# Optimization experiments

Hardware: AMD Instinct MI355X
Metric: run time of the kernel (lower is better)

## Reference

```python
import jax, jax.numpy as jnp
import numpy as np

KH, KW = 3, 3
STRIDE = (1, 1)
PAD = ((1, 1), (1, 1))
WEIGHT_BIT = 8


def asym_quant_params(num_bits, smin, smax):
    # ZeroQ asymmetric_linear_quantization_params (signed, integral zero point)
    n = 2.0 ** num_bits - 1.0
    scale = n / jnp.maximum(smax - smin, 1e-8)
    zero_point = jnp.round(scale * smin) + 2.0 ** (num_bits - 1)
    return scale, zero_point


def setup_inputs() -> dict:
    key = jax.random.key(0)
    k1, k2, k3 = jax.random.split(key, 3)
    x = jax.random.normal(k1, (16, 128, 56, 56), dtype=jnp.float32)
    weight = jax.random.normal(k2, (128, 128, 3, 3), dtype=jnp.float32) * 0.05
    bias = jax.random.normal(k3, (128,), dtype=jnp.float32) * 0.1
    return {"x": x, "weight": weight, "bias": bias, "activation_bit": 8}


def reference(x, weight, bias, activation_bit):
    B, C, H, W = x.shape
    Cout = weight.shape[0]

    # nn.functional.unfold(x, 3, stride=1, padding=1).transpose(1, 2)
    # conv_general_dilated_patches emits feature dim ordered (c, kh, kw),
    # matching torch unfold's channel-major layout.
    patches = jax.lax.conv_general_dilated_patches(
        x, filter_shape=(KH, KW), window_strides=STRIDE, padding=PAD)
    _, F, OH, OW = patches.shape          # F = C*KH*KW
    L = OH * OW
    calc_x = patches.reshape(B, F, L).transpose(0, 2, 1)  # [B, L, F]

    # ----- weight quantization: per-output-channel asymmetric int8 -----
    w2 = weight.reshape(Cout, -1)                          # [Cout, F]
    w_min = w2.min(axis=1)
    w_max = w2.max(axis=1)
    scale_w, zp_w = asym_quant_params(WEIGHT_BIT, w_min, w_max)  # [Cout]
    nw = 2.0 ** (WEIGHT_BIT - 1)
    qw = jnp.clip(jnp.round(scale_w[:, None] * w2 - zp_w[:, None]), -nw, nw - 1)

    # ----- activation quantization: per-tensor asymmetric -----
    x_min = calc_x.min()
    x_max = calc_x.max()
    scale_x, zp_x = asym_quant_params(activation_bit, x_min, x_max)
    nx = 2.0 ** (activation_bit - 1)
    qx = jnp.clip(jnp.round(scale_x * calc_x - zp_x), -nx, nx - 1)  # [B, L, F]

    # bias: linear_quantize(bias, scale_w*scale_x, 0)
    qb = jnp.round(scale_w * scale_x * bias)                # [Cout]

    # integer matmul + asymmetric zero-point correction
    # real value r ~= (q + zp) / scale, so
    # x.w*sx*sw = qx.qw + zp_w*sum(qx) + zp_x*sum(qw) + K*zp_w*zp_x
    mult_res = jnp.einsum('blf,of->blo', qx, qw)            # [B, L, Cout]
    K = w2.shape[1]
    res = (mult_res
           + zp_w * qx.sum(-1, keepdims=True)               # [B, L, 1]*[Cout]
           + zp_x * qw.sum(axis=1)                          # [Cout]
           + K * zp_w * zp_x
           + qb)                                            # [B, L, Cout]

    # requantize accumulator to activation_bit bits, then dequantize
    r_min, r_max = res.min(), res.max()
    scale_r, zp_r = asym_quant_params(activation_bit, r_min, r_max)
    nr = 2.0 ** (activation_bit - 1)
    qr = jnp.clip(jnp.round(scale_r * res - zp_r), -nr, nr - 1)
    out = (qr + zp_r) / scale_r / (scale_w * scale_x)       # [B, L, Cout]

    return out.transpose(0, 2, 1)                           # [B, Cout, L]
```

## Files before the change

### kernel.cpp

```cpp
#include <hip/hip_runtime.h>
#include <stdint.h>

#pragma clang fp contract(off)

typedef __attribute__((ext_vector_type(4))) int i32x4;
typedef __attribute__((ext_vector_type(16))) int i32x16;

#define B_    16
#define C_    128
#define HW_   56
#define L_    3136
#define CO_   128
#define F_    1152
#define M_    50176
#define NT_   784

#define OFF_PBMIN 0
#define OFF_PBMAX 3136
#define OFF_PRMIN 6272
#define OFF_PRMAX 9408
#define OFF_SW    12544
#define OFF_ZPW   13056
#define OFF_SXZX  13568
#define OFF_CNT   14080
#define OFF_QS    15616
#define OFF_QW    16384
#define OFF_QX    163840
#define OFF_S     6586368
#define OFF_RES   6787072

__device__ __forceinline__ int read_abit(const int* p) {
    int i = *p;
    if (i > 0 && i < 32) return i;
    float f = __int_as_float(i);
    int fi = (int)f;
    return (fi > 0 && fi < 32) ? fi : 8;
}

__device__ __forceinline__ int swz_tile(int blk) {
    return (blk & 7) * 98 + (blk >> 3);
}

__device__ __forceinline__ void gsync(char* ws, int sp) {
    unsigned* base = (unsigned*)(ws + OFF_CNT) + sp * 128;
    __syncthreads();
    if (threadIdx.x == 0) {
        __threadfence();
        atomicAdd(&base[(blockIdx.x & 7) * 16], 1u);
    }
    if (threadIdx.x < 8) {
        while (__hip_atomic_load(&base[threadIdx.x * 16],
                                 __ATOMIC_RELAXED, __HIP_MEMORY_SCOPE_AGENT) < 98u)
            __builtin_amdgcn_s_sleep(2);
    }
    __threadfence();
    __syncthreads();
}

__device__ __forceinline__ void block_fminmax(float& mn, float& mx, float* sred) {
    for (int m = 32; m; m >>= 1) {
        mn = fminf(mn, __shfl_xor(mn, m));
        mx = fmaxf(mx, __shfl_xor(mx, m));
    }
    int w = threadIdx.x >> 6;
    if ((threadIdx.x & 63) == 0) { sred[w] = mn; sred[4 + w] = mx; }
    __syncthreads();
    mn = fminf(fminf(sred[0], sred[1]), fminf(sred[2], sred[3]));
    mx = fmaxf(fmaxf(sred[4], sred[5]), fmaxf(sred[6], sred[7]));
    __syncthreads();
}
__device__ __forceinline__ void block_iminmax(int& mn, int& mx, int* ired) {
    for (int m = 32; m; m >>= 1) {
        mn = min(mn, __shfl_xor(mn, m));
        mx = max(mx, __shfl_xor(mx, m));
    }
    int w = threadIdx.x >> 6;
    if ((threadIdx.x & 63) == 0) { ired[w] = mn; ired[4 + w] = mx; }
    __syncthreads();
    mn = min(min(ired[0], ired[1]), min(ired[2], ired[3]));
    mx = max(max(ired[4], ired[5]), max(ired[6], ired[7]));
    __syncthreads();
}
__device__ __forceinline__ int block_isum(int v, int* ired) {
    for (int m = 32; m; m >>= 1) v += __shfl_xor(v, m);
    int w = threadIdx.x >> 6;
    if ((threadIdx.x & 63) == 0) ired[w] = v;
    __syncthreads();
    v = ired[0] + ired[1] + ired[2] + ired[3];
    __syncthreads();
    return v;
}

__global__ __launch_bounds__(256) void kA1(const float4* __restrict__ x4,
                                           char* __restrict__ ws) {
    __shared__ float sred[8];
    float mn = 0.0f, mx = 0.0f;
    int base = blockIdx.x * blockDim.x + threadIdx.x;
    int stride = NT_ * 256;
    #pragma unroll
    for (int k = 0; k < 8; ++k) {
        float4 v = x4[base + k * stride];
        mn = fminf(mn, fminf(fminf(v.x, v.y), fminf(v.z, v.w)));
        mx = fmaxf(mx, fmaxf(fmaxf(v.x, v.y), fmaxf(v.z, v.w)));
    }
    block_fminmax(mn, mx, sred);
    if (threadIdx.x == 0) {
        ((float*)(ws + OFF_PBMIN))[blockIdx.x] = mn;
        ((float*)(ws + OFF_PBMAX))[blockIdx.x] = mx;
    }
}

__global__ __launch_bounds__(256) void kA2(const float* __restrict__ wgt,
                                           const int* __restrict__ abit_p,
                                           char* __restrict__ ws) {
    __shared__ float sred[8];
    __shared__ int ired[8];
    if (blockIdx.x == CO_) {
        const float* pbmin = (const float*)(ws + OFF_PBMIN);
        const float* pbmax = (const float*)(ws + OFF_PBMAX);
        float mn = 0.0f, mx = 0.0f;
        for (int i = threadIdx.x; i < NT_; i += 256) {
            mn = fminf(mn, pbmin[i]);
            mx = fmaxf(mx, pbmax[i]);
        }
        block_fminmax(mn, mx, sred);
        if (threadIdx.x == 0) {
            int abit = read_abit(abit_p);
            float nlv = (float)((1 << abit) - 1);
            float sx = nlv / fmaxf(mx - mn, 1e-8f);
            float zx = rintf(sx * mn) + (float)(1 << (abit - 1));
            ((float*)(ws + OFF_SXZX))[0] = sx;
            ((float*)(ws + OFF_SXZX))[1] = zx;
        }
        return;
    }
    int o = blockIdx.x;
    const float* wr = wgt + o * F_;
    float mn = 3.4e38f, mx = -3.4e38f;
    for (int f = threadIdx.x; f < F_; f += 256) {
        float v = wr[f];
        mn = fminf(mn, v); mx = fmaxf(mx, v);
    }
    block_fminmax(mn, mx, sred);
    float sw = 255.0f / fmaxf(mx - mn, 1e-8f);
    float zw = rintf(sw * mn) + 128.0f;
    signed char* qw = (signed char*)(ws + OFF_QW);
    int qsum = 0;
    for (int f = threadIdx.x; f < F_; f += 256) {
        float q = fminf(fmaxf(rintf(sw * wr[f] - zw), -128.0f), 127.0f);
        int qi = (int)q;
        qsum += qi;
        int c = f / 9, j = f - c * 9;
        qw[j * 16384 + (c >> 4) * 2048 + (o << 4) + (c & 15)] = (signed char)qi;
    }
    qsum = block_isum(qsum, ired);
    if (threadIdx.x == 0) {
        ((int*)(ws + OFF_QS))[o]  = qsum;
        ((int*)(ws + OFF_ZPW))[o] = (int)zw;
        ((float*)(ws + OFF_SW))[o] = sw;
    }
}

__device__ __forceinline__ void dev_p2x(const float* __restrict__ x, char* ws, char* pool,
                                        float sx, float zx, int nx) {
    int (*ssum)[64] = (int(*)[64])pool;
    float lo = -(float)nx, hif = (float)(nx - 1);
    signed char* qxt = (signed char*)(ws + OFF_QX);
    int gid = swz_tile(blockIdx.x);
    int b = gid / 49, lcq = gid - b * 49;
    int l0 = lcq * 64;
    int t = threadIdx.x, lane = t & 63, cgp = t >> 6;
    int l = l0 + lane;
    const float* xb = x + ((size_t)b * C_) * L_ + l;
    int4* dst = (int4*)(qxt + ((size_t)(b * L_ + l)) * 128);
    int psum = 0;
    #pragma unroll
    for (int ii = 0; ii < 2; ++ii) {
        int c16 = (cgp + 4 * ii) * 16;
        int wds[4];
        #pragma unroll
        for (int k = 0; k < 4; ++k) {
            int wv = 0;
            #pragma unroll
            for (int e = 0; e < 4; ++e) {
                int c = c16 + 4 * k + e;
                float v = xb[(size_t)c * L_];
                int qi = (int)fminf(fmaxf(rintf(sx * v - zx), lo), hif);
                psum += qi;
                wv |= (qi & 255) << (8 * e);
            }
            wds[k] = wv;
        }
        int4 vv; vv.x = wds[0]; vv.y = wds[1]; vv.z = wds[2]; vv.w = wds[3];
        dst[c16 >> 4] = vv;
    }
    ssum[cgp][lane] = psum;
    __syncthreads();
    if (cgp == 0) {
        int* S = (int*)(ws + OFF_S);
        S[b * L_ + l] = ssum[0][lane] + ssum[1][lane] + ssum[2][lane] + ssum[3][lane];
    }
    __syncthreads();
}

template <bool WRITE_RES>
__device__ __forceinline__ void dev_p3(char* __restrict__ ws, char* pool, int* ired,
                                       const float* __restrict__ bias,
                                       int abit, float sx, float zx,
                                       i32x16& acc0, i32x16& acc1) {
    signed char* As = (signed char*)pool;
    signed char* Bs = (signed char*)(pool + 8192);
    int* S_s = (int*)(pool + 24576);
    int* sq  = (int*)(pool + 25504);
    const signed char* qxt = (const signed char*)(ws + OFF_QX);
    const signed char* qw  = (const signed char*)(ws + OFF_QW);
    const int* Sg  = (const int*)(ws + OFF_S);
    const int* zpw = (const int*)(ws + OFF_ZPW);

    int t = threadIdx.x;
    int mg = swz_tile(blockIdx.x) * 64;
    int b = mg / L_, l0 = mg - b * L_;
    int prow0 = l0 / HW_;
    int nx = 1 << (abit - 1);
    int q0 = min(max(-(int)zx, -nx), nx - 1);
    int pw = (q0 & 255) * 0x01010101;
    int4 pad4; pad4.x = pw; pad4.y = pw; pad4.z = pw; pad4.w = pw;
    int padS = C_ * q0;
    const signed char* qxtb = qxt + (size_t)b * L_ * 128;
    const int* Sb = Sg + b * L_;

    int chA = t & 7, rowA0 = t >> 3, rowA1 = rowA0 + 32;
    int li0 = l0 + rowA0, li1 = l0 + rowA1;
    int oh0 = li0 / HW_, ow0 = li0 - oh0 * HW_;
    int oh1 = li1 / HW_, ow1 = li1 - oh1 * HW_;

    int4 a0, a1, br0, br1, br2, br3;
    #define P3_LOAD_A(J) do {                                                          \
        int kh = (J) / 3 - 1, kw = (J) % 3 - 1;                                        \
        int ih = oh0 + kh, iw = ow0 + kw;                                              \
        a0 = ((unsigned)ih < HW_ && (unsigned)iw < HW_)                                \
             ? *(const int4*)(qxtb + ((ih * HW_ + iw) << 7) + (chA << 4)) : pad4;      \
        ih = oh1 + kh; iw = ow1 + kw;                                                  \
        a1 = ((unsigned)ih < HW_ && (unsigned)iw < HW_)                                \
             ? *(const int4*)(qxtb + ((ih * HW_ + iw) << 7) + (chA << 4)) : pad4;      \
    } while (0)
    #define P3_LOAD_B(J) do {                                                          \
        const int4* src = (const int4*)(qw + (J) * 16384);                             \
        br0 = src[t]; br1 = src[256 + t]; br2 = src[512 + t]; br3 = src[768 + t];      \
    } while (0)

    P3_LOAD_A(0); P3_LOAD_B(0);
    if (t < 232) {
        int ri = t / 58, c1 = t - ri * 58;
        int ih = prow0 - 1 + ri, iw = c1 - 1;
        S_s[t] = ((unsigned)ih < HW_ && (unsigned)iw < HW_) ? Sb[ih * HW_ + iw] : padS;
    }
    __syncthreads();
    if (t < 64) {
        int l = l0 + t;
        int oh = l / HW_, ow = l - oh * HW_;
        int ri = oh - prow0 + 1, ci = ow + 1;
        int s = 0;
        #pragma unroll
        for (int dr = -1; dr <= 1; ++dr)
            #pragma unroll
            for (int dc = -1; dc <= 1; ++dc)
                s += S_s[(ri + dr) * 58 + ci + dc];
        sq[t] = s;
    }

    int lane = t & 63, w = t >> 6;
    int wm = (w >> 1) << 5, wn = (w & 1) << 6;
    int r = lane & 31, hi = lane >> 5;
    #pragma unroll
    for (int i = 0; i < 16; ++i) { acc0[i] = 0; acc1[i] = 0; }

    #pragma unroll
    for (int j = 0; j < 9; ++j) {
        if (j > 0) __syncthreads();
        *(int4*)&As[(rowA0 << 7) + ((chA ^ (rowA0 & 7)) << 4)] = a0;
        *(int4*)&As[(rowA1 << 7) + ((chA ^ (rowA1 & 7)) << 4)] = a1;
        {
            int4* d = (int4*)Bs;
            d[t] = br0; d[256 + t] = br1; d[512 + t] = br2; d[768 + t] = br3;
        }
        if (j < 8) { P3_LOAD_A(j + 1); P3_LOAD_B(j + 1); }
        __syncthreads();
        i32x4 af[4], bf0[4], bf1[4];
        #pragma unroll
        for (int kk = 0; kk < 4; ++kk) {
            int ch2 = kk * 2 + hi, row = wm + r;
            af[kk]  = *(const i32x4*)&As[(row << 7) + ((ch2 ^ (row & 7)) << 4)];
            bf0[kk] = *(const i32x4*)&Bs[ch2 * 2048 + ((wn + r) << 4)];
            bf1[kk] = *(const i32x4*)&Bs[ch2 * 2048 + ((wn + 32 + r) << 4)];
        }
        #pragma unroll
        for (int kk = 0; kk < 4; ++kk) {
            acc0 = __builtin_amdgcn_mfma_i32_32x32x32_i8(af[kk], bf0[kk], acc0, 0, 0, 0);
            acc1 = __builtin_amdgcn_mfma_i32_32x32x32_i8(af[kk], bf1[kk], acc1, 0, 0, 0);
        }
    }
    #undef P3_LOAD_A
    #undef P3_LOAD_B

    int o0 = wn + r, o1 = wn + 32 + r;
    const int* qs = (const int*)(ws + OFF_QS);
    const float* swp = (const float*)(ws + OFF_SW);
    int zxi = (int)zx;
    int zw0 = zpw[o0], zw1 = zpw[o1];
    int c0 = zxi * qs[o0] + F_ * zw0 * zxi + (int)rintf(swp[o0] * sx * bias[o0]);
    int c1 = zxi * qs[o1] + F_ * zw1 * zxi + (int)rintf(swp[o1] * sx * bias[o1]);
    int lmin = INT32_MAX, lmax = INT32_MIN;
    int* resp = (int*)(ws + OFF_RES);
    #pragma unroll
    for (int g = 0; g < 16; ++g) {
        int row = wm + (g & 3) + ((g >> 2) << 3) + (hi << 2);
        int s = sq[row];
        int v0 = acc0[g] + zw0 * s + c0;
        int v1 = acc1[g] + zw1 * s + c1;
        acc0[g] = v0; acc1[g] = v1;
        lmin = min(lmin, min(v0, v1));
        lmax = max(lmax, max(v0, v1));
        if (WRITE_RES) {
            int m = mg + row;
            resp[m * CO_ + o0] = v0;
            resp[m * CO_ + o1] = v1;
        }
    }
    block_iminmax(lmin, lmax, ired);
    if (t == 0) {
        ((int*)(ws + OFF_PRMIN))[blockIdx.x] = lmin;
        ((int*)(ws + OFF_PRMAX))[blockIdx.x] = lmax;
    }
    __syncthreads();
}

__device__ __forceinline__ void dev_reduce_pr(const char* ws, int* ired,
                                              int& rmin, int& rmax) {
    const int* prmin = (const int*)(ws + OFF_PRMIN);
    const int* prmax = (const int*)(ws + OFF_PRMAX);
    int mn = INT32_MAX, mx = INT32_MIN;
    for (int i = threadIdx.x; i < NT_; i += 256) {
        mn = min(mn, prmin[i]);
        mx = max(mx, prmax[i]);
    }
    block_iminmax(mn, mx, ired);
    rmin = mn; rmax = mx;
}

__device__ __forceinline__ void dev_p4(const char* ws, char* pool, float* __restrict__ out,
                                       int abit, float sx, int rmin, int rmax,
                                       const i32x16& acc0, const i32x16& acc1) {
    const float* scale_w = (const float*)(ws + OFF_SW);
    float* tile = (float*)pool;
    int t = threadIdx.x;
    int mg = swz_tile(blockIdx.x) * 64;
    int b = mg / L_, l0 = mg - b * L_;
    int lane = t & 63, w = t >> 6;
    int wm = (w >> 1) << 5, wn = (w & 1) << 6;
    int r = lane & 31, hi = lane >> 5;
    int o0 = wn + r, o1 = wn + 32 + r;
    int nx = 1 << (abit - 1);
    float nlev = (float)((1 << abit) - 1);
    float rminf = (float)rmin, rmaxf = (float)rmax;
    float sr = nlev / fmaxf(rmaxf - rminf, 1e-8f);
    float zr = rintf(sr * rminf) + (float)nx;
    float lo = -(float)nx, hiq = (float)(nx - 1);
    float swsx0 = scale_w[o0] * sx, swsx1 = scale_w[o1] * sx;
    #pragma unroll
    for (int g = 0; g < 16; ++g) {
        int row = wm + (g & 3) + ((g >> 2) << 3) + (hi << 2);
        float qa = fminf(fmaxf(rintf(sr * (float)acc0[g] - zr), lo), hiq);
        float qb = fminf(fmaxf(rintf(sr * (float)acc1[g] - zr), lo), hiq);
        tile[row * 129 + o0] = ((qa + zr) / sr) / swsx0;
        tile[row * 129 + o1] = ((qb + zr) / sr) / swsx1;
    }
    __syncthreads();
    #pragma unroll
    for (int i = 0; i < 8; ++i) {
        int o = (t >> 4) + i * 16;
        int l4 = (t & 15) * 4;
        float4 f;
        #pragma unroll
        for (int jj = 0; jj < 4; ++jj)
            ((float*)&f)[jj] = tile[(l4 + jj) * 129 + o];
        *(float4*)(out + ((size_t)(b * CO_ + o)) * L_ + l0 + l4) = f;
    }
}

__global__ __launch_bounds__(256, 4) void kB(const float* __restrict__ x,
                                             const float* __restrict__ bias,
                                             const int* __restrict__ abit_p,
                                             char* __restrict__ ws,
                                             float* __restrict__ out) {
    __shared__ __align__(16) char pool[33280];
    __shared__ int ired[8];

    float sx = ((const float*)(ws + OFF_SXZX))[0];
    float zx = ((const float*)(ws + OFF_SXZX))[1];
    int abit = read_abit(abit_p);
    int nx = 1 << (abit - 1);

    dev_p2x(x, ws, pool, sx, zx, nx);
    gsync(ws, 0);

    i32x16 acc0, acc1;
    dev_p3<false>(ws, pool, ired, bias, abit, sx, zx, acc0, acc1);
    gsync(ws, 1);

    int rmin, rmax;
    dev_reduce_pr(ws, ired, rmin, rmax);
    dev_p4(ws, pool, out, abit, sx, rmin, rmax, acc0, acc1);
}

__global__ __launch_bounds__(256) void fbB1(const float* __restrict__ x,
                                            const int* __restrict__ abit_p,
                                            char* __restrict__ ws) {
    __shared__ __align__(16) char pool[1024];
    float sx = ((const float*)(ws + OFF_SXZX))[0];
    float zx = ((const float*)(ws + OFF_SXZX))[1];
    int abit = read_abit(abit_p);
    int nx = 1 << (abit - 1);
    dev_p2x(x, ws, pool, sx, zx, nx);
}

__global__ __launch_bounds__(256, 4) void fbB2(const float* __restrict__ bias,
                                               const int* __restrict__ abit_p,
                                               char* __restrict__ ws) {
    __shared__ __align__(16) char pool[25760];
    __shared__ int ired[8];
    float sx = ((const float*)(ws + OFF_SXZX))[0];
    float zx = ((const float*)(ws + OFF_SXZX))[1];
    int abit = read_abit(abit_p);
    i32x16 acc0, acc1;
    dev_p3<true>(ws, pool, ired, bias, abit, sx, zx, acc0, acc1);
}

__global__ __launch_bounds__(256) void fbB3(const int* __restrict__ abit_p,
                                            char* __restrict__ ws,
                                            float* __restrict__ out) {
    __shared__ int tile[64 * 65];
    __shared__ int ired[8];
    float sxv = ((const float*)(ws + OFF_SXZX))[0];
    int abit = read_abit(abit_p);
    float nlv = (float)((1 << abit) - 1);
    int rmin, rmax;
    dev_reduce_pr(ws, ired, rmin, rmax);

    const int* res = (const int*)(ws + OFF_RES);
    const float* scale_w = (const float*)(ws + OFF_SW);
    int t = threadIdx.x;
    int bid = blockIdx.x;
    int lcq = bid % 49; int tmp2 = bid / 49; int ocq = tmp2 & 1; int b = tmp2 >> 1;
    int l0 = lcq * 64, o0 = ocq * 64;

    const int* resb = res + ((size_t)(b * L_ + l0)) * CO_ + o0;
    #pragma unroll
    for (int i = 0; i < 4; ++i) {
        int lr = (t >> 4) + i * 16;
        int oc4 = (t & 15) * 4;
        int4 v = *(const int4*)(resb + lr * CO_ + oc4);
        int* d = &tile[lr * 65 + oc4];
        d[0] = v.x; d[1] = v.y; d[2] = v.z; d[3] = v.w;
    }
    int nxq = 1 << (abit - 1);
    float rminf = (float)rmin, rmaxf = (float)rmax;
    float sr = nlv / fmaxf(rmaxf - rminf, 1e-8f);
    float zr = rintf(sr * rminf) + (float)nxq;
    float lo = -(float)nxq, hiq = (float)(nxq - 1);
    __syncthreads();
    #pragma unroll
    for (int i = 0; i < 4; ++i) {
        int o = (t >> 4) + i * 16;
        int l4 = (t & 15) * 4;
        float swsx = scale_w[o0 + o] * sxv;
        float4 f;
        #pragma unroll
        for (int jj = 0; jj < 4; ++jj) {
            int rv = tile[(l4 + jj) * 65 + o];
            float q = fminf(fmaxf(rintf(sr * (float)rv - zr), lo), hiq);
            ((float*)&f)[jj] = ((q + zr) / sr) / swsx;
        }
        *(float4*)(out + ((size_t)(b * CO_ + o0 + o)) * L_ + l0 + l4) = f;
    }
}


extern "C" void kernel_launch(void* const* d_in, const int* in_sizes, int n_in,
                              void* d_out, int out_size, void* d_ws, size_t ws_size,
                              hipStream_t stream) {
    const float* x      = (const float*)d_in[0];
    const float* weight = (const float*)d_in[1];
    const float* bias   = (const float*)d_in[2];
    const int*   abit   = (const int*)d_in[3];
    float* out = (float*)d_out;
    char* ws = (char*)d_ws;

    int dev = 0;
    hipGetDevice(&dev);
    int ncu = 0;
    hipDeviceGetAttribute(&ncu, hipDeviceAttributeMultiprocessorCount, dev);
    int nb = 0;
    hipOccupancyMaxActiveBlocksPerMultiprocessor(&nb, (const void*)kB, 256, 0);

    kA1<<<NT_, 256, 0, stream>>>((const float4*)x, ws);
    kA2<<<CO_ + 1, 256, 0, stream>>>(weight, abit, ws);

    if (nb > 0 && (long)nb * (long)ncu >= NT_) {
        hipMemsetAsync(ws + OFF_CNT, 0, 1024, stream);
        kB<<<NT_, 256, 0, stream>>>(x, bias, abit, ws, out);
    } else {
        fbB1<<<NT_, 256, 0, stream>>>(x, abit, ws);
        fbB2<<<NT_, 256, 0, stream>>>(bias, abit, ws);
        fbB3<<<1568, 256, 0, stream>>>(abit, ws, out);
    }
}
```

Measured before the change: 54.63 us.

## Merge stats kernels and move activation quantization out of cooperative kernel

Merges the activation min/max kernel and the weight quantization kernel into a single launch. The final activation reduction now runs redundantly in every block of a separate quantize-x kernel. That kernel-boundary split replaces the first software grid barrier inside the persistent kernel, so the cooperative kernel holds only the GEMM and the dequant phase with one barrier. The exchange is an extra kernel launch plus 784 redundant reductions over 784 partials, in return for one fewer spin barrier and one fewer launch.

```diff
diff --git a/kernel.cpp b/kernel.cpp
--- a/kernel.cpp
+++ b/kernel.cpp
@@ -16,18 +16,18 @@
 #define NT_   784
 
 #define OFF_PBMIN 0
-#define OFF_PBMAX 3136
-#define OFF_PRMIN 6272
-#define OFF_PRMAX 9408
-#define OFF_SW    12544
-#define OFF_ZPW   13056
-#define OFF_SXZX  13568
-#define OFF_CNT   14080
-#define OFF_QS    15616
-#define OFF_QW    16384
-#define OFF_QX    163840
-#define OFF_S     6586368
-#define OFF_RES   6787072
+#define OFF_PBMAX 4096
+#define OFF_PRMIN 8192
+#define OFF_PRMAX 12288
+#define OFF_SW    16384
+#define OFF_ZPW   16896
+#define OFF_SXZX  17408
+#define OFF_CNT   17536
+#define OFF_QS    18048
+#define OFF_QW    18560
+#define OFF_QX    166016
+#define OFF_S     6588544
+#define OFF_RES   6789248
 
 __device__ __forceinline__ int read_abit(const int* p) {
     int i = *p;
@@ -41,8 +41,8 @@
     return (blk & 7) * 98 + (blk >> 3);
 }
 
-__device__ __forceinline__ void gsync(char* ws, int sp) {
-    unsigned* base = (unsigned*)(ws + OFF_CNT) + sp * 128;
+__device__ __forceinline__ void gsync(char* ws) {
+    unsigned* base = (unsigned*)(ws + OFF_CNT);
     __syncthreads();
     if (threadIdx.x == 0) {
         __threadfence();
@@ -91,50 +91,30 @@
     return v;
 }
 
-__global__ __launch_bounds__(256) void kA1(const float4* __restrict__ x4,
-                                           char* __restrict__ ws) {
-    __shared__ float sred[8];
-    float mn = 0.0f, mx = 0.0f;
-    int base = blockIdx.x * blockDim.x + threadIdx.x;
-    int stride = NT_ * 256;
-    #pragma unroll
-    for (int k = 0; k < 8; ++k) {
-        float4 v = x4[base + k * stride];
-        mn = fminf(mn, fminf(fminf(v.x, v.y), fminf(v.z, v.w)));
-        mx = fmaxf(mx, fmaxf(fmaxf(v.x, v.y), fmaxf(v.z, v.w)));
-    }
-    block_fminmax(mn, mx, sred);
-    if (threadIdx.x == 0) {
-        ((float*)(ws + OFF_PBMIN))[blockIdx.x] = mn;
-        ((float*)(ws + OFF_PBMAX))[blockIdx.x] = mx;
-    }
-}
-
-__global__ __launch_bounds__(256) void kA2(const float* __restrict__ wgt,
-                                           const int* __restrict__ abit_p,
-                                           char* __restrict__ ws) {
+__global__ __launch_bounds__(256) void kA(const float4* __restrict__ x4,
+                                          const float* __restrict__ wgt,
+                                          char* __restrict__ ws) {
     __shared__ float sred[8];
     __shared__ int ired[8];
-    if (blockIdx.x == CO_) {
-        const float* pbmin = (const float*)(ws + OFF_PBMIN);
-        const float* pbmax = (const float*)(ws + OFF_PBMAX);
+    int blk = blockIdx.x;
+    if (blk < NT_) {
         float mn = 0.0f, mx = 0.0f;
-        for (int i = threadIdx.x; i < NT_; i += 256) {
-            mn = fminf(mn, pbmin[i]);
-            mx = fmaxf(mx, pbmax[i]);
+        int base = blk * blockDim.x + threadIdx.x;
+        int stride = NT_ * 256;
+        #pragma unroll
+        for (int k = 0; k < 8; ++k) {
+            float4 v = x4[base + k * stride];
+            mn = fminf(mn, fminf(fminf(v.x, v.y), fminf(v.z, v.w)));
+            mx = fmaxf(mx, fmaxf(fmaxf(v.x, v.y), fmaxf(v.z, v.w)));
         }
         block_fminmax(mn, mx, sred);
         if (threadIdx.x == 0) {
-            int abit = read_abit(abit_p);
-            float nlv = (float)((1 << abit) - 1);
-            float sx = nlv / fmaxf(mx - mn, 1e-8f);
-            float zx = rintf(sx * mn) + (float)(1 << (abit - 1));
-            ((float*)(ws + OFF_SXZX))[0] = sx;
-            ((float*)(ws + OFF_SXZX))[1] = zx;
+            ((float*)(ws + OFF_PBMIN))[blk] = mn;
+            ((float*)(ws + OFF_PBMAX))[blk] = mx;
         }
         return;
     }
-    int o = blockIdx.x;
+    int o = blk - NT_;
     const float* wr = wgt + o * F_;
     float mn = 3.4e38f, mx = -3.4e38f;
     for (int f = threadIdx.x; f < F_; f += 256) {
@@ -161,9 +141,30 @@
     }
 }
 
-__device__ __forceinline__ void dev_p2x(const float* __restrict__ x, char* ws, char* pool,
-                                        float sx, float zx, int nx) {
-    int (*ssum)[64] = (int(*)[64])pool;
+__global__ __launch_bounds__(256) void kP2x(const float* __restrict__ x,
+                                            const int* __restrict__ abit_p,
+                                            char* __restrict__ ws) {
+    __shared__ float sred[8];
+    __shared__ int ssum[4][64];
+    float mn = 0.0f, mx = 0.0f;
+    {
+        const float* pbmin = (const float*)(ws + OFF_PBMIN);
+        const float* pbmax = (const float*)(ws + OFF_PBMAX);
+        for (int i = threadIdx.x; i < NT_; i += 256) {
+            mn = fminf(mn, pbmin[i]);
+            mx = fmaxf(mx, pbmax[i]);
+        }
+        block_fminmax(mn, mx, sred);
+    }
+    int abit = read_abit(abit_p);
+    float nlv = (float)((1 << abit) - 1);
+    float sx = nlv / fmaxf(mx - mn, 1e-8f);
+    float zx = rintf(sx * mn) + (float)(1 << (abit - 1));
+    if (threadIdx.x == 0 && blockIdx.x == 0) {
+        ((float*)(ws + OFF_SXZX))[0] = sx;
+        ((float*)(ws + OFF_SXZX))[1] = zx;
+    }
+    int nx = 1 << (abit - 1);
     float lo = -(float)nx, hif = (float)(nx - 1);
     signed char* qxt = (signed char*)(ws + OFF_QX);
     int gid = swz_tile(blockIdx.x);
@@ -200,7 +201,6 @@
         int* S = (int*)(ws + OFF_S);
         S[b * L_ + l] = ssum[0][lane] + ssum[1][lane] + ssum[2][lane] + ssum[3][lane];
     }
-    __syncthreads();
 }
 
 template <bool WRITE_RES>
@@ -348,11 +348,25 @@
     rmin = mn; rmax = mx;
 }
 
-__device__ __forceinline__ void dev_p4(const char* ws, char* pool, float* __restrict__ out,
-                                       int abit, float sx, int rmin, int rmax,
-                                       const i32x16& acc0, const i32x16& acc1) {
-    const float* scale_w = (const float*)(ws + OFF_SW);
-    float* tile = (float*)pool;
+__global__ __launch_bounds__(256, 4) void kCoop(const float* __restrict__ bias,
+                                                const int* __restrict__ abit_p,
+                                                char* __restrict__ ws,
+                                                float* __restrict__ out) {
+    __shared__ __align__(16) char pool[33280];
+    __shared__ int ired[8];
+
+    float sx = ((const float*)(ws + OFF_SXZX))[0];
+    float zx = ((const float*)(ws + OFF_SXZX))[1];
+    int abit = read_abit(abit_p);
+
+    i32x16 acc0, acc1;
+    dev_p3<false>(ws, pool, ired, bias, abit, sx, zx, acc0, acc1);
+    gsync(ws);
+
+    int rmin, rmax;
+    dev_reduce_pr(ws, ired, rmin, rmax);
+
+    const float* swp = (const float*)(ws + OFF_SW);
     int t = threadIdx.x;
     int mg = swz_tile(blockIdx.x) * 64;
     int b = mg / L_, l0 = mg - b * L_;
@@ -362,11 +376,11 @@
     int o0 = wn + r, o1 = wn + 32 + r;
     int nx = 1 << (abit - 1);
     float nlev = (float)((1 << abit) - 1);
-    float rminf = (float)rmin, rmaxf = (float)rmax;
-    float sr = nlev / fmaxf(rmaxf - rminf, 1e-8f);
-    float zr = rintf(sr * rminf) + (float)nx;
+    float sr = nlev / fmaxf((float)rmax - (float)rmin, 1e-8f);
+    float zr = rintf(sr * (float)rmin) + (float)nx;
     float lo = -(float)nx, hiq = (float)(nx - 1);
-    float swsx0 = scale_w[o0] * sx, swsx1 = scale_w[o1] * sx;
+    float swsx0 = swp[o0] * sx, swsx1 = swp[o1] * sx;
+    float* tile = (float*)pool;
     #pragma unroll
     for (int g = 0; g < 16; ++g) {
         int row = wm + (g & 3) + ((g >> 2) << 3) + (hi << 2);
@@ -388,45 +402,9 @@
     }
 }
 
-__global__ __launch_bounds__(256, 4) void kB(const float* __restrict__ x,
-                                             const float* __restrict__ bias,
-                                             const int* __restrict__ abit_p,
-                                             char* __restrict__ ws,
-                                             float* __restrict__ out) {
-    __shared__ __align__(16) char pool[33280];
-    __shared__ int ired[8];
-
-    float sx = ((const float*)(ws + OFF_SXZX))[0];
-    float zx = ((const float*)(ws + OFF_SXZX))[1];
-    int abit = read_abit(abit_p);
-    int nx = 1 << (abit - 1);
-
-    dev_p2x(x, ws, pool, sx, zx, nx);
-    gsync(ws, 0);
-
-    i32x16 acc0, acc1;
-    dev_p3<false>(ws, pool, ired, bias, abit, sx, zx, acc0, acc1);
-    gsync(ws, 1);
-
-    int rmin, rmax;
-    dev_reduce_pr(ws, ired, rmin, rmax);
-    dev_p4(ws, pool, out, abit, sx, rmin, rmax, acc0, acc1);
-}
-
-__global__ __launch_bounds__(256) void fbB1(const float* __restrict__ x,
-                                            const int* __restrict__ abit_p,
-                                            char* __restrict__ ws) {
-    __shared__ __align__(16) char pool[1024];
-    float sx = ((const float*)(ws + OFF_SXZX))[0];
-    float zx = ((const float*)(ws + OFF_SXZX))[1];
-    int abit = read_abit(abit_p);
-    int nx = 1 << (abit - 1);
-    dev_p2x(x, ws, pool, sx, zx, nx);
-}
-
-__global__ __launch_bounds__(256, 4) void fbB2(const float* __restrict__ bias,
-                                               const int* __restrict__ abit_p,
-                                               char* __restrict__ ws) {
+__global__ __launch_bounds__(256, 4) void fbGEMM(const float* __restrict__ bias,
+                                                 const int* __restrict__ abit_p,
+                                                 char* __restrict__ ws) {
     __shared__ __align__(16) char pool[25760];
     __shared__ int ired[8];
     float sx = ((const float*)(ws + OFF_SXZX))[0];
@@ -436,9 +414,9 @@
     dev_p3<true>(ws, pool, ired, bias, abit, sx, zx, acc0, acc1);
 }
 
-__global__ __launch_bounds__(256) void fbB3(const int* __restrict__ abit_p,
-                                            char* __restrict__ ws,
-                                            float* __restrict__ out) {
+__global__ __launch_bounds__(256) void fbDEQ(const int* __restrict__ abit_p,
+                                             char* __restrict__ ws,
+                                             float* __restrict__ out) {
     __shared__ int tile[64 * 65];
     __shared__ int ired[8];
     float sxv = ((const float*)(ws + OFF_SXZX))[0];
@@ -464,9 +442,8 @@
         d[0] = v.x; d[1] = v.y; d[2] = v.z; d[3] = v.w;
     }
     int nxq = 1 << (abit - 1);
-    float rminf = (float)rmin, rmaxf = (float)rmax;
-    float sr = nlv / fmaxf(rmaxf - rminf, 1e-8f);
-    float zr = rintf(sr * rminf) + (float)nxq;
+    float sr = nlv / fmaxf((float)rmax - (float)rmin, 1e-8f);
+    float zr = rintf(sr * (float)rmin) + (float)nxq;
     float lo = -(float)nxq, hiq = (float)(nxq - 1);
     __syncthreads();
     #pragma unroll
@@ -501,17 +478,16 @@
     int ncu = 0;
     hipDeviceGetAttribute(&ncu, hipDeviceAttributeMultiprocessorCount, dev);
     int nb = 0;
-    hipOccupancyMaxActiveBlocksPerMultiprocessor(&nb, (const void*)kB, 256, 0);
-
-    kA1<<<NT_, 256, 0, stream>>>((const float4*)x, ws);
-    kA2<<<CO_ + 1, 256, 0, stream>>>(weight, abit, ws);
+    hipOccupancyMaxActiveBlocksPerMultiprocessor(&nb, (const void*)kCoop, 256, 0);
+
+    kA<<<NT_ + CO_, 256, 0, stream>>>((const float4*)x, weight, ws);
+    kP2x<<<NT_, 256, 0, stream>>>(x, abit, ws);
 
     if (nb > 0 && (long)nb * (long)ncu >= NT_) {
-        hipMemsetAsync(ws + OFF_CNT, 0, 1024, stream);
-        kB<<<NT_, 256, 0, stream>>>(x, bias, abit, ws, out);
+        hipMemsetAsync(ws + OFF_CNT, 0, 512, stream);
+        kCoop<<<NT_, 256, 0, stream>>>(bias, abit, ws, out);
     } else {
-        fbB1<<<NT_, 256, 0, stream>>>(x, abit, ws);
-        fbB2<<<NT_, 256, 0, stream>>>(bias, abit, ws);
-        fbB3<<<1568, 256, 0, stream>>>(abit, ws, out);
-    }
-}
+        fbGEMM<<<NT_, 256, 0, stream>>>(bias, abit, ws);
+        fbDEQ<<<1568, 256, 0, stream>>>(abit, ws, out);
+    }
+}
```

Result: no change. 54.02 us, median of 2 (-1.1%).
